# Kernel tuning notes

Hardware: AMD Instinct MI355X
Metric: run time of the kernel (lower is better)

Reference implementation:

```python
import jax, jax.numpy as jnp
import numpy as np

DIM_IN1 = 512
DIM_IN2 = 512
DIM_OUT = 64


def setup_inputs() -> dict:
    key = jax.random.key(0)
    k1, k2, kw, kb = jax.random.split(key, 4)
    B, L = 8, 256
    inputs1 = jax.random.normal(k1, (B, L, DIM_IN1), dtype=jnp.float32)
    inputs2 = jax.random.normal(k2, (B, L, DIM_IN2), dtype=jnp.float32)
    # nn.Bilinear init: U(-1/sqrt(in1_features), 1/sqrt(in1_features))
    bound = 1.0 / np.sqrt(DIM_IN1)
    weight = jax.random.uniform(kw, (DIM_OUT, DIM_IN1, DIM_IN2), dtype=jnp.float32,
                                minval=-bound, maxval=bound)
    bias = jax.random.uniform(kb, (DIM_OUT,), dtype=jnp.float32,
                              minval=-bound, maxval=bound)
    return {"inputs1": inputs1, "inputs2": inputs2, "weight": weight, "bias": bias}


def reference(inputs1, inputs2, weight, bias):
    # out[b,i,j,k] = sum_{p,q} x1[b,i,p] * W[k,p,q] * x2[b,j,q] + bias[k]
    # Two smaller batched matmuls instead of materializing [B,L,L,D] expansions.
    tmp = jnp.einsum('bip,kpq->bikq', inputs1, weight)   # [B, L, K, D2]
    out = jnp.einsum('bikq,bjq->bijk', tmp, inputs2)      # [B, L, L, K]
    return out + bias
```

## Files before the change

### kernel.cpp

```cpp
#include <hip/hip_runtime.h>
#include <stdint.h>


typedef __bf16 bf16x8 __attribute__((ext_vector_type(8)));
typedef float  f32x4  __attribute__((ext_vector_type(4)));

#define KDIM 512
#define BM 256
#define BN 128
#define BK 64
#define ABYTES 32768
#define BBYTES 16384
#define BUFB   49152

__global__ __launch_bounds__(256) void f32_to_bf16_kernel(
    const float* __restrict__ in, __bf16* __restrict__ out, long n8)
{
    for (long i = blockIdx.x * 256L + threadIdx.x; i < n8; i += gridDim.x * 256L) {
        f32x4 a = *(const f32x4*)(in + i * 8);
        f32x4 b = *(const f32x4*)(in + i * 8 + 4);
        bf16x8 o;
        o[0]=(__bf16)a[0]; o[1]=(__bf16)a[1]; o[2]=(__bf16)a[2]; o[3]=(__bf16)a[3];
        o[4]=(__bf16)b[0]; o[5]=(__bf16)b[1]; o[6]=(__bf16)b[2]; o[7]=(__bf16)b[3];
        *(bf16x8*)(out + i * 8) = o;
    }
}

#define VMW(N) do { \
    asm volatile("s_waitcnt vmcnt(" #N ")" ::: "memory"); \
    __builtin_amdgcn_sched_barrier(0); } while (0)
#define LGKM0() do { \
    asm volatile("s_waitcnt lgkmcnt(0)" ::: "memory"); \
    __builtin_amdgcn_sched_barrier(0); } while (0)
#define SB() __builtin_amdgcn_sched_barrier(0)

#define LG0(kt) do { \
    e0 = *(const bf16x8*)(gA + (kt) * BK); \
    e1 = *(const bf16x8*)(gA + 64L * KDIM + (kt) * BK); \
    e2 = *(const bf16x8*)(gB + (kt) * BK); } while (0)
#define LG1(kt) do { \
    o0 = *(const bf16x8*)(gA + 128L * KDIM + (kt) * BK); \
    o1 = *(const bf16x8*)(gA + 192L * KDIM + (kt) * BK); \
    o2 = *(const bf16x8*)(gB + 64L * KDIM + (kt) * BK); } while (0)
#define WG0(bi) do { char* w_ = lds + (bi) * BUFB; \
    *(bf16x8*)(w_ + sbw)              = e0; \
    *(bf16x8*)(w_ + 8192 + sbw)       = e1; \
    *(bf16x8*)(w_ + ABYTES + sbw)     = e2; } while (0)
#define WG1(bi) do { char* w_ = lds + (bi) * BUFB; \
    *(bf16x8*)(w_ + 16384 + sbw)          = o0; \
    *(bf16x8*)(w_ + 24576 + sbw)          = o1; \
    *(bf16x8*)(w_ + ABYTES + 8192 + sbw)  = o2; } while (0)

#define RDB(bi) do { const char* b_ = lds + (bi) * BUFB + ABYTES; \
    _Pragma("unroll") for (int j_ = 0; j_ < 4; ++j_) { \
        const int ro_ = (wn * 64 + j_ * 16 + lcol) * 128; \
        bfr[j_][0] = *(const bf16x8*)(b_ + ro_ + ko0); \
        bfr[j_][1] = *(const bf16x8*)(b_ + ro_ + ko1); } } while (0)
#define RDA(bi, ih) do { const char* a_ = lds + (bi) * BUFB; \
    _Pragma("unroll") for (int i_ = 0; i_ < 2; ++i_) { \
        const int ro_ = (wm * 64 + ((ih) * 2 + i_) * 16 + lcol) * 128; \
        af[i_][0] = *(const bf16x8*)(a_ + ro_ + ko0); \
        af[i_][1] = *(const bf16x8*)(a_ + ro_ + ko1); } } while (0)
#define MF(ih) do { \
    _Pragma("unroll") for (int i_ = 0; i_ < 2; ++i_) \
    _Pragma("unroll") for (int j_ = 0; j_ < 4; ++j_) \
    _Pragma("unroll") for (int k_ = 0; k_ < 2; ++k_) \
        acc[(ih) * 2 + i_][j_] = __builtin_amdgcn_mfma_f32_16x16x32_bf16( \
            af[i_][k_], bfr[j_][k_], acc[(ih) * 2 + i_][j_], 0, 0, 0); } while (0)

template <typename OutT>
__global__ __launch_bounds__(512, 2) void gemm_nt_256x128(
    const __bf16* __restrict__ A,
    const __bf16* __restrict__ B,
    OutT* __restrict__ C,
    const float* __restrict__ bias,
    int ldc, int mtiles,
    long sA, long sB, long sC)
{
    __shared__ __align__(16) char lds[2 * BUFB];

    const int tid  = threadIdx.x;
    const int lane = tid & 63;
    const int wave = tid >> 6;
    const int wm   = wave & 3;
    const int wn   = wave >> 2;
    const int lcol = lane & 15;
    const int krow = (lane >> 4) & 3;
    const int rsw  = (lcol & 7) << 4;
    const int ko0  = (krow * 16) ^ rsw;
    const int ko1  = (64 + krow * 16) ^ rsw;

    long flat = (long)blockIdx.z * gridDim.x + blockIdx.x;
    long nwg  = (long)gridDim.x * gridDim.z;
    long q = nwg >> 3, r8 = nwg & 7;
    long xcd = flat & 7, lo = flat >> 3;
    long sz = (xcd < r8 ? xcd * (q + 1) : r8 * (q + 1) + (xcd - r8) * q) + lo;
    const int z   = (int)(sz / (long)gridDim.x);
    const int rem = (int)(sz % (long)gridDim.x);
    const int n0 = (rem / mtiles) * BN;
    const int m0 = (rem % mtiles) * BM;

    A += (long)z * sA + (long)m0 * KDIM;
    B += (long)z * sB + (long)n0 * KDIM;
    C += (long)z * sC;

    const int r  = tid >> 3;
    const int c8 = tid & 7;
    const int sbw = r * 128 + ((c8 * 16) ^ ((r & 7) << 4));
    const __bf16* gA = A + (long)r * KDIM + c8 * 8;
    const __bf16* gB = B + (long)r * KDIM + c8 * 8;

    bf16x8 e0, e1, e2, o0, o1, o2;
    f32x4 acc[4][4] = {};

    LG0(0); LG1(0);
    VMW(3); WG0(0); LG0(1);
    VMW(3); WG1(0); LG1(1);
    LGKM0();
    __builtin_amdgcn_s_barrier(); SB();

#pragma unroll
    for (int t = 0; t < 6; ++t) {
        const int cur = t & 1, nxt = cur ^ 1;
        bf16x8 bfr[4][2], af[2][2];
        RDB(cur); RDA(cur, 0);
        VMW(3); WG0(nxt); LG0(t + 2); SB();
        __builtin_amdgcn_s_setprio(1); MF(0); __builtin_amdgcn_s_setprio(0); SB();
        RDA(cur, 1);
        VMW(3); WG1(nxt); LG1(t + 2); SB();
        __builtin_amdgcn_s_setprio(1); MF(1); __builtin_amdgcn_s_setprio(0);
        LGKM0();
        __builtin_amdgcn_s_barrier(); SB();
    }
    {
        bf16x8 bfr[4][2], af[2][2];
        RDB(0); RDA(0, 0);
        VMW(3); WG0(1); SB();
        __builtin_amdgcn_s_setprio(1); MF(0); __builtin_amdgcn_s_setprio(0); SB();
        RDA(0, 1);
        VMW(0); WG1(1); SB();
        __builtin_amdgcn_s_setprio(1); MF(1); __builtin_amdgcn_s_setprio(0);
        LGKM0();
        __builtin_amdgcn_s_barrier(); SB();
    }
    {
        bf16x8 bfr[4][2], af[2][2];
        RDB(1); RDA(1, 0); MF(0);
        RDA(1, 1);         MF(1);
    }

    float badd[4];
#pragma unroll
    for (int j = 0; j < 4; ++j)
        badd[j] = bias ? bias[j * 16 + lcol] : 0.f;
#pragma unroll
    for (int i = 0; i < 4; ++i) {
#pragma unroll
        for (int rr = 0; rr < 4; ++rr) {
            const int row = m0 + wm * 64 + i * 16 + krow * 4 + rr;
            OutT* cp = C + (long)row * ldc + n0 + wn * 64 + lcol;
#pragma unroll
            for (int j = 0; j < 4; ++j)
                cp[j * 16] = (OutT)(acc[i][j][rr] + badd[j]);
        }
    }
}

extern "C" void kernel_launch(void* const* d_in, const int* in_sizes, int n_in,
                              void* d_out, int out_size, void* d_ws, size_t ws_size,
                              hipStream_t stream)
{
    (void)in_sizes; (void)n_in; (void)out_size;
    const float* x1f = (const float*)d_in[0];
    const float* x2f = (const float*)d_in[1];
    const float* Wf  = (const float*)d_in[2];
    const float* bs  = (const float*)d_in[3];
    float* out = (float*)d_out;

    const long N_W = 64L * 512 * 512;
    const long N_X = 8L * 256 * 512;
    __bf16* Wb  = (__bf16*)d_ws;
    __bf16* x1b = Wb + N_W;
    __bf16* x2b = x1b + N_X;
    __bf16* S   = x2b + N_X;
    const size_t head_bytes = (size_t)(N_W + 2 * N_X) * sizeof(__bf16);

    f32_to_bf16_kernel<<<2048, 256, 0, stream>>>(Wf,  Wb,  N_W / 8);
    f32_to_bf16_kernel<<<512,  256, 0, stream>>>(x1f, x1b, N_X / 8);
    f32_to_bf16_kernel<<<512,  256, 0, stream>>>(x2f, x2b, N_X / 8);

    const long ROWS_TOTAL = 2048;
    const long ROW_ELEMS  = 32768;

    long rows_chunk = (ws_size > head_bytes)
        ? (long)((ws_size - head_bytes) / (ROW_ELEMS * sizeof(__bf16))) : 0;
    rows_chunk &= ~255L;
    if (rows_chunk < 256) rows_chunk = 256;
    if (rows_chunk > ROWS_TOTAL) rows_chunk = ROWS_TOTAL;

    for (long r0 = 0; r0 < ROWS_TOTAL; r0 += rows_chunk) {
        long rows = ROWS_TOTAL - r0;
        if (rows > rows_chunk) rows = rows_chunk;
        long nbc = rows >> 8;
        int  mt  = (int)(rows >> 8);

        dim3 gA((unsigned)((32768 / BN) * mt), 1, 1);
        gemm_nt_256x128<__bf16><<<gA, 512, 0, stream>>>(
            x2b + r0 * KDIM, Wb, S, nullptr, 32768, mt, 0, 0, 0);

        dim3 gB2(16384 / BN, 1, (unsigned)nbc);
        gemm_nt_256x128<float><<<gB2, 512, 0, stream>>>(
            x1b + r0 * KDIM,
            S,
            out + r0 * 16384,
            bs, 16384, 1,
            256L * KDIM, 256L * ROW_ELEMS, 256L * 16384);
    }
}
```

Measured before the change: 334.7 us.

## Halve GEMM K-tile to shrink LDS and raise occupancy to four blocks

```diff
diff --git a/kernel.cpp b/kernel.cpp
--- a/kernel.cpp
+++ b/kernel.cpp
@@ -8,10 +8,10 @@
 #define KDIM 512
 #define BM 256
 #define BN 128
-#define BK 64
-#define ABYTES 32768
-#define BBYTES 16384
-#define BUFB   49152
+#define BK 32
+#define NKT (KDIM / BK)
+#define ABYTES 16384
+#define BUFB   24576
 
 __global__ __launch_bounds__(256) void f32_to_bf16_kernel(
     const float* __restrict__ in, __bf16* __restrict__ out, long n8)
@@ -34,42 +34,31 @@
     __builtin_amdgcn_sched_barrier(0); } while (0)
 #define SB() __builtin_amdgcn_sched_barrier(0)
 
-#define LG0(kt) do { \
+#define LG(kt) do { \
     e0 = *(const bf16x8*)(gA + (kt) * BK); \
-    e1 = *(const bf16x8*)(gA + 64L * KDIM + (kt) * BK); \
+    e1 = *(const bf16x8*)(gA + 128L * KDIM + (kt) * BK); \
     e2 = *(const bf16x8*)(gB + (kt) * BK); } while (0)
-#define LG1(kt) do { \
-    o0 = *(const bf16x8*)(gA + 128L * KDIM + (kt) * BK); \
-    o1 = *(const bf16x8*)(gA + 192L * KDIM + (kt) * BK); \
-    o2 = *(const bf16x8*)(gB + 64L * KDIM + (kt) * BK); } while (0)
-#define WG0(bi) do { char* w_ = lds + (bi) * BUFB; \
-    *(bf16x8*)(w_ + sbw)              = e0; \
-    *(bf16x8*)(w_ + 8192 + sbw)       = e1; \
-    *(bf16x8*)(w_ + ABYTES + sbw)     = e2; } while (0)
-#define WG1(bi) do { char* w_ = lds + (bi) * BUFB; \
-    *(bf16x8*)(w_ + 16384 + sbw)          = o0; \
-    *(bf16x8*)(w_ + 24576 + sbw)          = o1; \
-    *(bf16x8*)(w_ + ABYTES + 8192 + sbw)  = o2; } while (0)
+#define WG(bi) do { char* w_ = lds + (bi) * BUFB; \
+    *(bf16x8*)(w_ + sbw)          = e0; \
+    *(bf16x8*)(w_ + 8192 + sbw)   = e1; \
+    *(bf16x8*)(w_ + ABYTES + sbw) = e2; } while (0)
 
 #define RDB(bi) do { const char* b_ = lds + (bi) * BUFB + ABYTES; \
-    _Pragma("unroll") for (int j_ = 0; j_ < 4; ++j_) { \
-        const int ro_ = (wn * 64 + j_ * 16 + lcol) * 128; \
-        bfr[j_][0] = *(const bf16x8*)(b_ + ro_ + ko0); \
-        bfr[j_][1] = *(const bf16x8*)(b_ + ro_ + ko1); } } while (0)
-#define RDA(bi, ih) do { const char* a_ = lds + (bi) * BUFB; \
-    _Pragma("unroll") for (int i_ = 0; i_ < 2; ++i_) { \
-        const int ro_ = (wm * 64 + ((ih) * 2 + i_) * 16 + lcol) * 128; \
-        af[i_][0] = *(const bf16x8*)(a_ + ro_ + ko0); \
-        af[i_][1] = *(const bf16x8*)(a_ + ro_ + ko1); } } while (0)
-#define MF(ih) do { \
-    _Pragma("unroll") for (int i_ = 0; i_ < 2; ++i_) \
     _Pragma("unroll") for (int j_ = 0; j_ < 4; ++j_) \
-    _Pragma("unroll") for (int k_ = 0; k_ < 2; ++k_) \
-        acc[(ih) * 2 + i_][j_] = __builtin_amdgcn_mfma_f32_16x16x32_bf16( \
-            af[i_][k_], bfr[j_][k_], acc[(ih) * 2 + i_][j_], 0, 0, 0); } while (0)
+        bfr[j_] = *(const bf16x8*)(b_ + (wn * 64 + j_ * 16 + lcol) * 64 + ko); \
+    } while (0)
+#define RDA(bi) do { const char* a_ = lds + (bi) * BUFB; \
+    _Pragma("unroll") for (int i_ = 0; i_ < 4; ++i_) \
+        af[i_] = *(const bf16x8*)(a_ + (wm * 64 + i_ * 16 + lcol) * 64 + ko); \
+    } while (0)
+#define MF() do { \
+    _Pragma("unroll") for (int i_ = 0; i_ < 4; ++i_) \
+    _Pragma("unroll") for (int j_ = 0; j_ < 4; ++j_) \
+        acc[i_][j_] = __builtin_amdgcn_mfma_f32_16x16x32_bf16( \
+            af[i_], bfr[j_], acc[i_][j_], 0, 0, 0); } while (0)
 
 template <typename OutT>
-__global__ __launch_bounds__(512, 2) void gemm_nt_256x128(
+__global__ __launch_bounds__(512, 4) void gemm_nt_r5(
     const __bf16* __restrict__ A,
     const __bf16* __restrict__ B,
     OutT* __restrict__ C,
@@ -86,9 +75,7 @@
     const int wn   = wave >> 2;
     const int lcol = lane & 15;
     const int krow = (lane >> 4) & 3;
-    const int rsw  = (lcol & 7) << 4;
-    const int ko0  = (krow * 16) ^ rsw;
-    const int ko1  = (64 + krow * 16) ^ rsw;
+    const int ko   = (krow * 16) ^ ((lcol & 3) << 4);
 
     long flat = (long)blockIdx.z * gridDim.x + blockIdx.x;
     long nwg  = (long)gridDim.x * gridDim.z;
@@ -104,49 +91,56 @@
     B += (long)z * sB + (long)n0 * KDIM;
     C += (long)z * sC;
 
-    const int r  = tid >> 3;
-    const int c8 = tid & 7;
-    const int sbw = r * 128 + ((c8 * 16) ^ ((r & 7) << 4));
-    const __bf16* gA = A + (long)r * KDIM + c8 * 8;
-    const __bf16* gB = B + (long)r * KDIM + c8 * 8;
-
-    bf16x8 e0, e1, e2, o0, o1, o2;
+    const int r  = tid >> 2;
+    const int c4 = tid & 3;
+    const int sbw = r * 64 + ((c4 * 16) ^ ((r & 3) << 4));
+    const __bf16* gA = A + (long)r * KDIM + c4 * 8;
+    const __bf16* gB = B + (long)r * KDIM + c4 * 8;
+
+    bf16x8 e0, e1, e2;
     f32x4 acc[4][4] = {};
 
-    LG0(0); LG1(0);
-    VMW(3); WG0(0); LG0(1);
-    VMW(3); WG1(0); LG1(1);
+    LG(0);
+    {   bf16x8 t0 = e0, t1 = e1, t2 = e2;
+        LG(1);
+        VMW(3);
+        char* w_ = lds;
+        *(bf16x8*)(w_ + sbw)          = t0;
+        *(bf16x8*)(w_ + 8192 + sbw)   = t1;
+        *(bf16x8*)(w_ + ABYTES + sbw) = t2;
+    }
     LGKM0();
     __builtin_amdgcn_s_barrier(); SB();
 
 #pragma unroll
-    for (int t = 0; t < 6; ++t) {
+    for (int t = 0; t < NKT - 2; ++t) {
         const int cur = t & 1, nxt = cur ^ 1;
-        bf16x8 bfr[4][2], af[2][2];
-        RDB(cur); RDA(cur, 0);
-        VMW(3); WG0(nxt); LG0(t + 2); SB();
-        __builtin_amdgcn_s_setprio(1); MF(0); __builtin_amdgcn_s_setprio(0); SB();
-        RDA(cur, 1);
-        VMW(3); WG1(nxt); LG1(t + 2); SB();
-        __builtin_amdgcn_s_setprio(1); MF(1); __builtin_amdgcn_s_setprio(0);
+        bf16x8 bfr[4], af[4];
+        RDB(cur); RDA(cur);
+        {   bf16x8 p0 = e0, p1 = e1, p2 = e2;
+            LG(t + 2);
+            VMW(3);
+            char* w_ = lds + nxt * BUFB;
+            *(bf16x8*)(w_ + sbw)          = p0;
+            *(bf16x8*)(w_ + 8192 + sbw)   = p1;
+            *(bf16x8*)(w_ + ABYTES + sbw) = p2;
+        }
+        SB();
+        __builtin_amdgcn_s_setprio(1); MF(); __builtin_amdgcn_s_setprio(0);
         LGKM0();
         __builtin_amdgcn_s_barrier(); SB();
     }
     {
-        bf16x8 bfr[4][2], af[2][2];
-        RDB(0); RDA(0, 0);
-        VMW(3); WG0(1); SB();
-        __builtin_amdgcn_s_setprio(1); MF(0); __builtin_amdgcn_s_setprio(0); SB();
-        RDA(0, 1);
-        VMW(0); WG1(1); SB();
-        __builtin_amdgcn_s_setprio(1); MF(1); __builtin_amdgcn_s_setprio(0);
+        bf16x8 bfr[4], af[4];
+        RDB(0); RDA(0);
+        VMW(0); WG(1); SB();
+        __builtin_amdgcn_s_setprio(1); MF(); __builtin_amdgcn_s_setprio(0);
         LGKM0();
         __builtin_amdgcn_s_barrier(); SB();
     }
     {
-        bf16x8 bfr[4][2], af[2][2];
-        RDB(1); RDA(1, 0); MF(0);
-        RDA(1, 1);         MF(1);
+        bf16x8 bfr[4], af[4];
+        RDB(1); RDA(1); MF();
     }
 
     float badd[4];
@@ -205,11 +199,11 @@
         int  mt  = (int)(rows >> 8);
 
         dim3 gA((unsigned)((32768 / BN) * mt), 1, 1);
-        gemm_nt_256x128<__bf16><<<gA, 512, 0, stream>>>(
+        gemm_nt_r5<__bf16><<<gA, 512, 0, stream>>>(
             x2b + r0 * KDIM, Wb, S, nullptr, 32768, mt, 0, 0, 0);
 
         dim3 gB2(16384 / BN, 1, (unsigned)nbc);
-        gemm_nt_256x128<float><<<gB2, 512, 0, stream>>>(
+        gemm_nt_r5<float><<<gB2, 512, 0, stream>>>(
             x1b + r0 * KDIM,
             S,
             out + r0 * 16384,
```

New measurement: 409.1 us. 22.2% more time.

## Replace double-buffered LDS pipeline with single buffer and higher occupancy

Applied to the files above, without the earlier changes.

```diff
diff --git a/kernel.cpp b/kernel.cpp
--- a/kernel.cpp
+++ b/kernel.cpp
@@ -9,9 +9,9 @@
 #define BM 256
 #define BN 128
 #define BK 64
+#define NKT (KDIM / BK)
 #define ABYTES 32768
-#define BBYTES 16384
-#define BUFB   49152
+#define LDSB   49152
 
 __global__ __launch_bounds__(256) void f32_to_bf16_kernel(
     const float* __restrict__ in, __bf16* __restrict__ out, long n8)
@@ -26,50 +26,42 @@
     }
 }
 
-#define VMW(N) do { \
-    asm volatile("s_waitcnt vmcnt(" #N ")" ::: "memory"); \
-    __builtin_amdgcn_sched_barrier(0); } while (0)
 #define LGKM0() do { \
     asm volatile("s_waitcnt lgkmcnt(0)" ::: "memory"); \
     __builtin_amdgcn_sched_barrier(0); } while (0)
 #define SB() __builtin_amdgcn_sched_barrier(0)
+#define BAR() do { __builtin_amdgcn_s_barrier(); SB(); } while (0)
 
-#define LG0(kt) do { \
+#define LG(kt) do { \
     e0 = *(const bf16x8*)(gA + (kt) * BK); \
     e1 = *(const bf16x8*)(gA + 64L * KDIM + (kt) * BK); \
-    e2 = *(const bf16x8*)(gB + (kt) * BK); } while (0)
-#define LG1(kt) do { \
-    o0 = *(const bf16x8*)(gA + 128L * KDIM + (kt) * BK); \
-    o1 = *(const bf16x8*)(gA + 192L * KDIM + (kt) * BK); \
-    o2 = *(const bf16x8*)(gB + 64L * KDIM + (kt) * BK); } while (0)
-#define WG0(bi) do { char* w_ = lds + (bi) * BUFB; \
-    *(bf16x8*)(w_ + sbw)              = e0; \
-    *(bf16x8*)(w_ + 8192 + sbw)       = e1; \
-    *(bf16x8*)(w_ + ABYTES + sbw)     = e2; } while (0)
-#define WG1(bi) do { char* w_ = lds + (bi) * BUFB; \
-    *(bf16x8*)(w_ + 16384 + sbw)          = o0; \
-    *(bf16x8*)(w_ + 24576 + sbw)          = o1; \
-    *(bf16x8*)(w_ + ABYTES + 8192 + sbw)  = o2; } while (0)
+    e2 = *(const bf16x8*)(gA + 128L * KDIM + (kt) * BK); \
+    e3 = *(const bf16x8*)(gA + 192L * KDIM + (kt) * BK); \
+    f0 = *(const bf16x8*)(gB + (kt) * BK); \
+    f1 = *(const bf16x8*)(gB + 64L * KDIM + (kt) * BK); } while (0)
+#define WG() do { \
+    *(bf16x8*)(lds + sbw)                  = e0; \
+    *(bf16x8*)(lds + 8192 + sbw)           = e1; \
+    *(bf16x8*)(lds + 16384 + sbw)          = e2; \
+    *(bf16x8*)(lds + 24576 + sbw)          = e3; \
+    *(bf16x8*)(lds + ABYTES + sbw)         = f0; \
+    *(bf16x8*)(lds + ABYTES + 8192 + sbw)  = f1; } while (0)
 
-#define RDB(bi) do { const char* b_ = lds + (bi) * BUFB + ABYTES; \
-    _Pragma("unroll") for (int j_ = 0; j_ < 4; ++j_) { \
-        const int ro_ = (wn * 64 + j_ * 16 + lcol) * 128; \
-        bfr[j_][0] = *(const bf16x8*)(b_ + ro_ + ko0); \
-        bfr[j_][1] = *(const bf16x8*)(b_ + ro_ + ko1); } } while (0)
-#define RDA(bi, ih) do { const char* a_ = lds + (bi) * BUFB; \
-    _Pragma("unroll") for (int i_ = 0; i_ < 2; ++i_) { \
-        const int ro_ = (wm * 64 + ((ih) * 2 + i_) * 16 + lcol) * 128; \
-        af[i_][0] = *(const bf16x8*)(a_ + ro_ + ko0); \
-        af[i_][1] = *(const bf16x8*)(a_ + ro_ + ko1); } } while (0)
-#define MF(ih) do { \
-    _Pragma("unroll") for (int i_ = 0; i_ < 2; ++i_) \
-    _Pragma("unroll") for (int j_ = 0; j_ < 4; ++j_) \
-    _Pragma("unroll") for (int k_ = 0; k_ < 2; ++k_) \
-        acc[(ih) * 2 + i_][j_] = __builtin_amdgcn_mfma_f32_16x16x32_bf16( \
-            af[i_][k_], bfr[j_][k_], acc[(ih) * 2 + i_][j_], 0, 0, 0); } while (0)
+#define COMPUTE() do { \
+    _Pragma("unroll") for (int kk_ = 0; kk_ < 2; ++kk_) { \
+        const int ko_ = (kk_ * 64 + krow * 16) ^ rsw; \
+        bf16x8 bfr[4]; \
+        _Pragma("unroll") for (int j_ = 0; j_ < 4; ++j_) \
+            bfr[j_] = *(const bf16x8*)(lds + ABYTES + (wn * 64 + j_ * 16 + lcol) * 128 + ko_); \
+        _Pragma("unroll") for (int i_ = 0; i_ < 4; ++i_) { \
+            bf16x8 af = *(const bf16x8*)(lds + (wm * 64 + i_ * 16 + lcol) * 128 + ko_); \
+            _Pragma("unroll") for (int j_ = 0; j_ < 4; ++j_) \
+                acc[i_][j_] = __builtin_amdgcn_mfma_f32_16x16x32_bf16( \
+                    af, bfr[j_], acc[i_][j_], 0, 0, 0); \
+        } } } while (0)
 
 template <typename OutT>
-__global__ __launch_bounds__(512, 2) void gemm_nt_256x128(
+__global__ __launch_bounds__(512, 4) void gemm_nt_r6(
     const __bf16* __restrict__ A,
     const __bf16* __restrict__ B,
     OutT* __restrict__ C,
@@ -77,7 +69,7 @@
     int ldc, int mtiles,
     long sA, long sB, long sC)
 {
-    __shared__ __align__(16) char lds[2 * BUFB];
+    __shared__ __align__(16) char lds[LDSB];
 
     const int tid  = threadIdx.x;
     const int lane = tid & 63;
@@ -87,8 +79,6 @@
     const int lcol = lane & 15;
     const int krow = (lane >> 4) & 3;
     const int rsw  = (lcol & 7) << 4;
-    const int ko0  = (krow * 16) ^ rsw;
-    const int ko1  = (64 + krow * 16) ^ rsw;
 
     long flat = (long)blockIdx.z * gridDim.x + blockIdx.x;
     long nwg  = (long)gridDim.x * gridDim.z;
@@ -110,44 +100,25 @@
     const __bf16* gA = A + (long)r * KDIM + c8 * 8;
     const __bf16* gB = B + (long)r * KDIM + c8 * 8;
 
-    bf16x8 e0, e1, e2, o0, o1, o2;
+    bf16x8 e0, e1, e2, e3, f0, f1;
     f32x4 acc[4][4] = {};
 
-    LG0(0); LG1(0);
-    VMW(3); WG0(0); LG0(1);
-    VMW(3); WG1(0); LG1(1);
+    LG(0);
+    WG();
     LGKM0();
-    __builtin_amdgcn_s_barrier(); SB();
+    BAR();
 
 #pragma unroll
-    for (int t = 0; t < 6; ++t) {
-        const int cur = t & 1, nxt = cur ^ 1;
-        bf16x8 bfr[4][2], af[2][2];
-        RDB(cur); RDA(cur, 0);
-        VMW(3); WG0(nxt); LG0(t + 2); SB();
-        __builtin_amdgcn_s_setprio(1); MF(0); __builtin_amdgcn_s_setprio(0); SB();
-        RDA(cur, 1);
-        VMW(3); WG1(nxt); LG1(t + 2); SB();
-        __builtin_amdgcn_s_setprio(1); MF(1); __builtin_amdgcn_s_setprio(0);
+    for (int t = 0; t < NKT - 1; ++t) {
+        LG(t + 1); SB();
+        COMPUTE();
         LGKM0();
-        __builtin_amdgcn_s_barrier(); SB();
+        BAR();
+        WG();
+        LGKM0();
+        BAR();
     }
-    {
-        bf16x8 bfr[4][2], af[2][2];
-        RDB(0); RDA(0, 0);
-        VMW(3); WG0(1); SB();
-        __builtin_amdgcn_s_setprio(1); MF(0); __builtin_amdgcn_s_setprio(0); SB();
-        RDA(0, 1);
-        VMW(0); WG1(1); SB();
-        __builtin_amdgcn_s_setprio(1); MF(1); __builtin_amdgcn_s_setprio(0);
-        LGKM0();
-        __builtin_amdgcn_s_barrier(); SB();
-    }
-    {
-        bf16x8 bfr[4][2], af[2][2];
-        RDB(1); RDA(1, 0); MF(0);
-        RDA(1, 1);         MF(1);
-    }
+    COMPUTE();
 
     float badd[4];
 #pragma unroll
@@ -205,11 +176,11 @@
         int  mt  = (int)(rows >> 8);
 
         dim3 gA((unsigned)((32768 / BN) * mt), 1, 1);
-        gemm_nt_256x128<__bf16><<<gA, 512, 0, stream>>>(
+        gemm_nt_r6<__bf16><<<gA, 512, 0, stream>>>(
             x2b + r0 * KDIM, Wb, S, nullptr, 32768, mt, 0, 0, 0);
 
         dim3 gB2(16384 / BN, 1, (unsigned)nbc);
-        gemm_nt_256x128<float><<<gB2, 512, 0, stream>>>(
+        gemm_nt_r6<float><<<gB2, 512, 0, stream>>>(
             x1b + r0 * KDIM,
             S,
             out + r0 * 16384,
```

Result: faster. 323.0 us (-3.5%).
